# Optimization experiments

Hardware: AMD Instinct MI355X
Metric: run time of the kernel (lower is better)

Reference implementation:

```python
import jax, jax.numpy as jnp
import numpy as np

B, N, D, M = 8, 8192, 256, 2  # M from init_kwargs


def setup_inputs() -> dict:
    key = jax.random.key(0)
    ks = jax.random.split(key, 10)
    g_names = ['G_l_ii', 'G_l_ij', 'G_l_ji', 'G_l_jj', 'G_u_ii', 'G_u_ij', 'G_u_ji', 'G_u_jj']
    inp = {'input': jax.random.normal(ks[0], (B, N, D), dtype=jnp.float32)}
    for i, name in enumerate(g_names):
        inp[name] = jax.random.normal(ks[1 + i], (B, N - 1), dtype=jnp.float32)
    inp['Diag'] = jax.random.normal(ks[9], (B, N), dtype=jnp.float32)
    inp['transform'] = 1
    return inp


def _banded_sweep(x, a0, b0, lo, dm, hi, aL, bL):
    # One tridiagonal Givens sweep over axis 1 of x [B,N,D].
    # row 0:       a0*x[0]   + b0*x[1]
    # rows 1..N-2: lo*x[i-1] + dm*x[i] + hi*x[i+1]
    # row N-1:     aL*x[N-2] + bL*x[N-1]
    n = x.shape[1]
    y0 = a0[:, None, None] * x[:, 0:1] + b0[:, None, None] * x[:, 1:2]
    ym = (lo[:, :, None] * x[:, :-2]
          + dm[:, :, None] * x[:, 1:n - 1]
          + hi[:, :, None] * x[:, 2:])
    yl = aL[:, None, None] * x[:, n - 2:n - 1] + bL[:, None, None] * x[:, n - 1:n]
    return jnp.concatenate([y0, ym, yl], axis=1)


def _forward(x, gl_ii, gl_ij, gl_ji, gl_jj, gu_ii, gu_ij, gu_ji, gu_jj, diag, transform):
    b, n, d = x.shape
    if transform:
        # stride permutation (only defined for even N in the original)
        x = x.reshape(b, n // M, M, d).transpose(0, 2, 1, 3).reshape(b, n, d)
    else:
        x = diag[:, :, None] * x
    # upper sweep -> Y
    y = _banded_sweep(
        x,
        gu_ii[:, 0], gu_ij[:, 0],
        gu_ji[:, :-1], gu_jj[:, :-1] * gu_ii[:, 1:], gu_jj[:, :-1] * gu_ij[:, 1:],
        gu_ji[:, n - 2], gu_jj[:, n - 2])
    # lower sweep -> Z
    z = _banded_sweep(
        y,
        gl_ii[:, 0], gl_ij[:, 0],
        gl_ii[:, 1:] * gl_ji[:, :-1], gl_ii[:, 1:] * gl_jj[:, :-1], gl_ij[:, 1:],
        gl_ji[:, n - 2], gl_jj[:, n - 2])
    if transform:
        z = diag[:, :, None] * z
    else:
        z = z.reshape(b, n // M, M, d).transpose(0, 2, 1, 3).reshape(b, n, d)
    return z


def reference(input, G_l_ii, G_l_ij, G_l_ji, G_l_jj, G_u_ii, G_u_ij, G_u_ji, G_u_jj, Diag, transform):
    return _forward(input, G_l_ii, G_l_ij, G_l_ji, G_l_jj,
                    G_u_ii, G_u_ij, G_u_ji, G_u_jj, Diag, transform)
```

## Files before the change

### kernel.cpp

```cpp
#include <hip/hip_runtime.h>

#define NN 8192
#define DD 256
#define NH (NN / 2)
#define BB 8
#define RPW 8
#define WPB 4
#define NBLK (BB * NN / RPW / WPB)
#define CPX (NBLK / 8)

__device__ __forceinline__ float4 f4_load(const float* p) {
    return *reinterpret_cast<const float4*>(p);
}
__device__ __forceinline__ float4 f4_scale(float s, float4 v) {
    return make_float4(s * v.x, s * v.y, s * v.z, s * v.w);
}
__device__ __forceinline__ float4 f4_fma(float s, float4 v, float4 a) {
    return make_float4(fmaf(s, v.x, a.x), fmaf(s, v.y, a.y),
                       fmaf(s, v.z, a.z), fmaf(s, v.w, a.w));
}

__global__ __launch_bounds__(256, 4) void dhhp_kernel(
    const float* __restrict__ x,
    const float* __restrict__ gl_ii, const float* __restrict__ gl_ij,
    const float* __restrict__ gl_ji, const float* __restrict__ gl_jj,
    const float* __restrict__ gu_ii, const float* __restrict__ gu_ij,
    const float* __restrict__ gu_ji, const float* __restrict__ gu_jj,
    const float* __restrict__ diag, const int* __restrict__ transform,
    float* __restrict__ out)
{
    const int bid  = blockIdx.x;
    const int swz  = (bid & 7) * CPX + (bid >> 3);
    int wid = swz * WPB + (threadIdx.x >> 6);
    wid = __builtin_amdgcn_readfirstlane(wid);
    const int b    = wid >> 10;
    const int j0   = (wid & 1023) << 3;
    const int col  = (threadIdx.x & 63) << 2;
    const int tr   = *transform;

    const float* xb  = x    + (size_t)b * NN * DD;
    const float* db  = diag + (size_t)b * NN;
    const float* uii = gu_ii + (size_t)b * (NN - 1);
    const float* uij = gu_ij + (size_t)b * (NN - 1);
    const float* uji = gu_ji + (size_t)b * (NN - 1);
    const float* ujj = gu_jj + (size_t)b * (NN - 1);
    const float* lii = gl_ii + (size_t)b * (NN - 1);
    const float* lij = gl_ij + (size_t)b * (NN - 1);
    const float* lji = gl_ji + (size_t)b * (NN - 1);
    const float* ljj = gl_jj + (size_t)b * (NN - 1);
    float* ob = out + (size_t)b * NN * DD;

    auto permRow = [&](int i) -> int {
        return tr ? ((i < NH) ? (i << 1) : (((i - NH) << 1) | 1)) : i;
    };
    auto loadRowI = [&](int i) -> float4 {
        float4 v = f4_load(xb + (size_t)permRow(i) * DD + col);
        if (!tr) v = f4_scale(db[i], v);
        return v;
    };
    auto loadRowC = [&](int i) -> float4 {
        int ic = i < 0 ? 0 : (i > NN - 1 ? NN - 1 : i);
        return loadRowI(ic);
    };
    auto yInner = [&](int i, float4 xm, float4 xc, float4 xp) -> float4 {
        float lo  = uji[i - 1];
        float cjj = ujj[i - 1];
        float dm  = cjj * uii[i];
        float hi  = cjj * uij[i];
        float4 r = f4_scale(lo, xm);
        r = f4_fma(dm, xc, r);
        r = f4_fma(hi, xp, r);
        return r;
    };
    auto yAny = [&](int i, float4 xm, float4 xc, float4 xp) -> float4 {
        int ic = i < 0 ? 0 : (i > NN - 1 ? NN - 1 : i);
        if (ic == 0)      return f4_fma(uii[0], xc, f4_scale(uij[0], xp));
        if (ic == NN - 1) return f4_fma(uji[NN - 2], xm, f4_scale(ujj[NN - 2], xc));
        return yInner(ic, xm, xc, xp);
    };
    auto zInner = [&](int j, float4 ym, float4 yc, float4 yp) -> float4 {
        float ci = lii[j];
        float lo = ci * lji[j - 1];
        float dm = ci * ljj[j - 1];
        float hi = lij[j];
        float4 r = f4_scale(lo, ym);
        r = f4_fma(dm, yc, r);
        r = f4_fma(hi, yp, r);
        return r;
    };
    auto zAny = [&](int j, float4 ym, float4 yc, float4 yp) -> float4 {
        if (j == 0)      return f4_fma(lii[0], yc, f4_scale(lij[0], yp));
        if (j == NN - 1) return f4_fma(lji[NN - 2], ym, f4_scale(ljj[NN - 2], yc));
        return zInner(j, ym, yc, yp);
    };
    auto storeRow = [&](int j, float4 z) {
        int jo;
        float4 o;
        if (tr) { o = f4_scale(db[j], z); jo = j; }
        else    { o = z; jo = (j & 1) ? (NH + (j >> 1)) : (j >> 1); }
        *reinterpret_cast<float4*>(ob + (size_t)jo * DD + col) = o;
    };

    const bool interior = (j0 >= 2) && (j0 <= NN - RPW - 2);

    float4 xr[RPW + 4];
    float4 yr[RPW + 2];

    if (interior) {
        #pragma unroll
        for (int t = 0; t < RPW + 4; ++t) xr[t] = loadRowI(j0 - 2 + t);
        #pragma unroll
        for (int t = 0; t < RPW + 2; ++t)
            yr[t] = yInner(j0 - 1 + t, xr[t], xr[t + 1], xr[t + 2]);
        #pragma unroll
        for (int t = 0; t < RPW; ++t)
            storeRow(j0 + t, zInner(j0 + t, yr[t], yr[t + 1], yr[t + 2]));
    } else {
        #pragma unroll
        for (int t = 0; t < RPW + 4; ++t) xr[t] = loadRowC(j0 - 2 + t);
        #pragma unroll
        for (int t = 0; t < RPW + 2; ++t)
            yr[t] = yAny(j0 - 1 + t, xr[t], xr[t + 1], xr[t + 2]);
        #pragma unroll
        for (int t = 0; t < RPW; ++t)
            storeRow(j0 + t, zAny(j0 + t, yr[t], yr[t + 1], yr[t + 2]));
    }
}

extern "C" void kernel_launch(void* const* d_in, const int* in_sizes, int n_in,
                              void* d_out, int out_size, void* d_ws, size_t ws_size,
                              hipStream_t stream) {
    const float* x     = (const float*)d_in[0];
    const float* gl_ii = (const float*)d_in[1];
    const float* gl_ij = (const float*)d_in[2];
    const float* gl_ji = (const float*)d_in[3];
    const float* gl_jj = (const float*)d_in[4];
    const float* gu_ii = (const float*)d_in[5];
    const float* gu_ij = (const float*)d_in[6];
    const float* gu_ji = (const float*)d_in[7];
    const float* gu_jj = (const float*)d_in[8];
    const float* diag  = (const float*)d_in[9];
    const int* transform = (const int*)d_in[10];
    float* out = (float*)d_out;

    dim3 grid(NBLK);
    dim3 block(256);
    hipLaunchKernelGGL(dhhp_kernel, grid, block, 0, stream,
                       x, gl_ii, gl_ij, gl_ji, gl_jj,
                       gu_ii, gu_ij, gu_ji, gu_jj, diag, transform, out);
}
```

Before: 30.43 us.

## Stage block-wide x halo tile in LDS via direct global-to-LDS loads

Each block of four waves now cooperatively loads a shared 36-row tile of x into LDS with global_load_lds, instead of each wave loading its own 12-row window. The goal is to cut redundant halo reads from global memory and issue them asynchronously. In exchange it adds a block barrier and 36KB of LDS per block, which may limit occupancy, and drops the min-blocks launch bound.

```diff
diff --git a/kernel.cpp b/kernel.cpp
--- a/kernel.cpp
+++ b/kernel.cpp
@@ -6,12 +6,11 @@
 #define BB 8
 #define RPW 8
 #define WPB 4
-#define NBLK (BB * NN / RPW / WPB)
+#define RPB (RPW * WPB)
+#define SROWS (RPB + 4)
+#define NBLK (BB * NN / RPB)
 #define CPX (NBLK / 8)
 
-__device__ __forceinline__ float4 f4_load(const float* p) {
-    return *reinterpret_cast<const float4*>(p);
-}
 __device__ __forceinline__ float4 f4_scale(float s, float4 v) {
     return make_float4(s * v.x, s * v.y, s * v.z, s * v.w);
 }
@@ -20,7 +19,7 @@
                        fmaf(s, v.z, a.z), fmaf(s, v.w, a.w));
 }
 
-__global__ __launch_bounds__(256, 4) void dhhp_kernel(
+__global__ __launch_bounds__(256) void dhhp_kernel(
     const float* __restrict__ x,
     const float* __restrict__ gl_ii, const float* __restrict__ gl_ij,
     const float* __restrict__ gl_ji, const float* __restrict__ gl_jj,
@@ -29,14 +28,15 @@
     const float* __restrict__ diag, const int* __restrict__ transform,
     float* __restrict__ out)
 {
-    const int bid  = blockIdx.x;
-    const int swz  = (bid & 7) * CPX + (bid >> 3);
-    int wid = swz * WPB + (threadIdx.x >> 6);
-    wid = __builtin_amdgcn_readfirstlane(wid);
-    const int b    = wid >> 10;
-    const int j0   = (wid & 1023) << 3;
-    const int col  = (threadIdx.x & 63) << 2;
-    const int tr   = *transform;
+    __shared__ float smem[SROWS * DD];
+
+    const int bid = blockIdx.x;
+    const int swz = (bid & 7) * CPX + (bid >> 3);
+    const int b   = swz >> 8;
+    const int j0b = (swz & 255) << 5;
+    const int w   = __builtin_amdgcn_readfirstlane(threadIdx.x >> 6);
+    const int col = (threadIdx.x & 63) << 2;
+    const int tr  = *transform;
 
     const float* xb  = x    + (size_t)b * NN * DD;
     const float* db  = diag + (size_t)b * NN;
@@ -50,17 +50,30 @@
     const float* ljj = gl_jj + (size_t)b * (NN - 1);
     float* ob = out + (size_t)b * NN * DD;
 
-    auto permRow = [&](int i) -> int {
-        return tr ? ((i < NH) ? (i << 1) : (((i - NH) << 1) | 1)) : i;
-    };
-    auto loadRowI = [&](int i) -> float4 {
-        float4 v = f4_load(xb + (size_t)permRow(i) * DD + col);
-        if (!tr) v = f4_scale(db[i], v);
+    #pragma unroll
+    for (int q = 0; q < SROWS / WPB; ++q) {
+        const int s  = w + q * WPB;
+        const int i  = j0b - 2 + s;
+        const int ic = i < 0 ? 0 : (i > NN - 1 ? NN - 1 : i);
+        const int r  = tr ? ((ic < NH) ? (ic << 1) : (((ic - NH) << 1) | 1)) : ic;
+        const float* gp = xb + (size_t)r * DD + col;
+        float*       lp = smem + s * DD;
+        __builtin_amdgcn_global_load_lds(
+            (const __attribute__((address_space(1))) void*)gp,
+            (__attribute__((address_space(3))) void*)lp, 16, 0, 0);
+    }
+    __syncthreads();
+
+    const int j0 = j0b + (w << 3);
+
+    auto xRow = [&](int i) -> float4 {
+        const int s = i - (j0b - 2);
+        float4 v = *reinterpret_cast<const float4*>(smem + s * DD + col);
+        if (!tr) {
+            const int ic = i < 0 ? 0 : (i > NN - 1 ? NN - 1 : i);
+            v = f4_scale(db[ic], v);
+        }
         return v;
-    };
-    auto loadRowC = [&](int i) -> float4 {
-        int ic = i < 0 ? 0 : (i > NN - 1 ? NN - 1 : i);
-        return loadRowI(ic);
     };
     auto yInner = [&](int i, float4 xm, float4 xc, float4 xp) -> float4 {
         float lo  = uji[i - 1];
@@ -101,14 +114,14 @@
         *reinterpret_cast<float4*>(ob + (size_t)jo * DD + col) = o;
     };
 
-    const bool interior = (j0 >= 2) && (j0 <= NN - RPW - 2);
-
     float4 xr[RPW + 4];
     float4 yr[RPW + 2];
 
+    const bool interior = (j0 >= 2) && (j0 <= NN - RPW - 2);
+
     if (interior) {
         #pragma unroll
-        for (int t = 0; t < RPW + 4; ++t) xr[t] = loadRowI(j0 - 2 + t);
+        for (int t = 0; t < RPW + 4; ++t) xr[t] = xRow(j0 - 2 + t);
         #pragma unroll
         for (int t = 0; t < RPW + 2; ++t)
             yr[t] = yInner(j0 - 1 + t, xr[t], xr[t + 1], xr[t + 2]);
@@ -117,7 +130,7 @@
             storeRow(j0 + t, zInner(j0 + t, yr[t], yr[t + 1], yr[t + 2]));
     } else {
         #pragma unroll
-        for (int t = 0; t < RPW + 4; ++t) xr[t] = loadRowC(j0 - 2 + t);
+        for (int t = 0; t < RPW + 4; ++t) xr[t] = xRow(j0 - 2 + t);
         #pragma unroll
         for (int t = 0; t < RPW + 2; ++t)
             yr[t] = yAny(j0 - 1 + t, xr[t], xr[t + 1], xr[t + 2]);
```

Measured after the change: 31.41 us. +3.2%, slower.
